# Optimization experiments

Measured on AMD Instinct MI355X. Metric: run time of the kernel, lower is better.

Reference implementation:

```python
import jax, jax.numpy as jnp
import numpy as np
import math

N_EMBD = 1024
N_HEAD = 16
N_CTX = 2048
SCALE = True
NEG = 1e10


def setup_inputs() -> dict:
    key = jax.random.key(0)
    ks = jax.random.split(key, 4)
    B, S = 2, 2048
    x = jax.random.normal(ks[0], (B, S, N_EMBD), dtype=jnp.float32)
    c_attn_w = jax.random.normal(ks[1], (N_EMBD, 3 * N_EMBD), dtype=jnp.float32) * 0.02
    c_attn_b = jnp.zeros((3 * N_EMBD,), dtype=jnp.float32)
    c_proj_w = jax.random.normal(ks[2], (N_EMBD, N_EMBD), dtype=jnp.float32) * 0.02
    c_proj_b = jnp.zeros((N_EMBD,), dtype=jnp.float32)
    return {"x": x, "c_attn_w": c_attn_w, "c_attn_b": c_attn_b,
            "c_proj_w": c_proj_w, "c_proj_b": c_proj_b}


def reference(x, c_attn_w, c_attn_b, c_proj_w, c_proj_b):
    B, S, D = x.shape
    H = N_HEAD
    hd = D // H
    qkv = x @ c_attn_w + c_attn_b                      # [B,S,3D]
    q, k, v = jnp.split(qkv, 3, axis=-1)
    # split heads -> [B,H,S,hd]
    q = q.reshape(B, S, H, hd).transpose(0, 2, 1, 3)
    k = k.reshape(B, S, H, hd).transpose(0, 2, 1, 3)
    v = v.reshape(B, S, H, hd).transpose(0, 2, 1, 3)
    w = jnp.einsum('bhqd,bhkd->bhqk', q, k)           # [B,H,S,S]
    if SCALE:
        w = w / math.sqrt(hd)
    # multiplicative causal mask trick: w*b - 1e10*(1-b)
    b = jnp.tril(jnp.ones((S, S), dtype=w.dtype))[None, None]
    w = w * b - NEG * (1.0 - b)
    w = jax.nn.softmax(w, axis=-1)
    a = jnp.einsum('bhqk,bhkd->bhqd', w, v)           # [B,H,S,hd]
    a = a.transpose(0, 2, 1, 3).reshape(B, S, D)      # merge heads
    a = a @ c_proj_w + c_proj_b
    present = jnp.stack((k, v))                       # [2,B,H,S,hd]
    return a, present
```

## Files before the change

kernel.cpp:

```cpp
#include <hip/hip_runtime.h>
#include <hip/hip_bf16.h>
#include <cstdint>
#include <cstddef>

#define SEQ 2048
#define DMODEL 1024
#define NHEAD 16
#define HDIM 64
#define MTOT 4096
#define NQKV 3072
#define KDIM 1024

#define OUT_K_BASE  4194304u
#define OUT_V_BASE  8388608u

#define QSCALE 0.18033688011112043f

typedef __attribute__((ext_vector_type(4))) float f32x4;
typedef __attribute__((ext_vector_type(8))) __bf16 bf16x8;
typedef __attribute__((ext_vector_type(8))) short s16x8;
typedef __attribute__((ext_vector_type(4))) short s16x4;
typedef __attribute__((ext_vector_type(2))) int i32x2;

static __device__ __forceinline__ unsigned short f2bf(float f) {
  unsigned int u = __builtin_bit_cast(unsigned int, f);
  u += 0x7FFFu + ((u >> 16) & 1u);
  return (unsigned short)(u >> 16);
}

static __device__ __forceinline__ float bf2f(unsigned short u) {
  unsigned int x = ((unsigned int)u) << 16;
  return __builtin_bit_cast(float, x);
}

static __device__ __forceinline__ s16x4 pack4(float4 v) {
  s16x4 r;
  r[0] = (short)f2bf(v.x);
  r[1] = (short)f2bf(v.y);
  r[2] = (short)f2bf(v.z);
  r[3] = (short)f2bf(v.w);
  return r;
}

static __device__ __forceinline__ int cvtpk(float lo, float hi) {
  int r;
  asm("v_cvt_pk_bf16_f32 %0, %1, %2" : "=v"(r) : "v"(lo), "v"(hi));
  return r;
}

static __device__ __forceinline__ f32x4 mfma16(s16x8 a, s16x8 b, f32x4 c) {
  return __builtin_amdgcn_mfma_f32_16x16x32_bf16(
      __builtin_bit_cast(bf16x8, a), __builtin_bit_cast(bf16x8, b), c, 0, 0, 0);
}

static __device__ __forceinline__ void gload16(const void* g, void* l) {
  __builtin_amdgcn_global_load_lds(
      (const __attribute__((address_space(1))) unsigned int*)(uintptr_t)g,
      (__attribute__((address_space(3))) unsigned int*)(uintptr_t)l,
      16, 0, 0);
}

#define WAITVM(n) asm volatile("s_waitcnt vmcnt(" #n ")" ::: "memory")

__global__ __launch_bounds__(256) void convert_x(
    const float* __restrict__ X, unsigned short* __restrict__ Xbf)
{
  int i = blockIdx.x * 256 + threadIdx.x;
  float4 v = reinterpret_cast<const float4*>(X)[i];
  reinterpret_cast<s16x4*>(Xbf)[i] = pack4(v);
}

__global__ __launch_bounds__(256) void convert_wt(
    const float* __restrict__ W, unsigned short* __restrict__ Wt, int N)
{
  __shared__ unsigned short t[64][72];
  const int n0 = blockIdx.x * 64, k0 = blockIdx.y * 64;
  const int tid = threadIdx.x;
#pragma unroll
  for (int i = 0; i < 4; ++i) {
    int f = tid + (i << 8);
    int r = f >> 4, c4 = (f & 15) << 2;
    float4 v = *reinterpret_cast<const float4*>(&W[(size_t)(k0 + r) * N + n0 + c4]);
    *reinterpret_cast<s16x4*>(&t[r][c4]) = pack4(v);
  }
  __syncthreads();
#pragma unroll
  for (int i = 0; i < 2; ++i) {
    int g = tid + (i << 8);
    int n = g >> 3, k8 = (g & 7) << 3;
    s16x8 o;
#pragma unroll
    for (int jj = 0; jj < 8; ++jj) o[jj] = (short)t[k8 + jj][n];
    *reinterpret_cast<s16x8*>(&Wt[(size_t)(n0 + n) * KDIM + k0 + k8]) = o;
  }
}

__global__ __launch_bounds__(256) void qkv_gemm(
    const unsigned short* __restrict__ Xbf,
    const unsigned short* __restrict__ Wt,
    const float* __restrict__ Bias,
    unsigned short* __restrict__ Qbf,
    unsigned short* __restrict__ Kbf,
    unsigned short* __restrict__ Vt)
{
  __shared__ __align__(16) unsigned short lds_a[2][128][64];
  __shared__ __align__(16) unsigned short lds_b[2][128][64];

  const int tid = threadIdx.x;
  const int lane = tid & 63;
  const int wv = tid >> 6;
  const int wr = wv >> 1, wc = wv & 1;
  const int m0 = blockIdx.x * 128;
  const int n0 = blockIdx.y * 128;
  const int lr = lane & 15;
  const int gq = lane >> 4;

  const f32x4 fzero = {0.f, 0.f, 0.f, 0.f};
  f32x4 acc[4][4];
#pragma unroll
  for (int i = 0; i < 4; ++i)
#pragma unroll
    for (int j = 0; j < 4; ++j) acc[i][j] = fzero;

  {
    const int r0 = tid >> 3;
    const int c0 = tid & 7;
    auto stage = [&](int nb, int kk) {
#pragma unroll
      for (int i = 0; i < 4; ++i) {
        int r = r0 + (i << 5);
        int sc = ((c0 ^ (r & 7)) << 3);
        int ub = (((i << 8) + (wv << 6)) << 3);
        gload16(&Xbf[(size_t)(m0 + r) * KDIM + kk + sc], &lds_a[nb][0][0] + ub);
        gload16(&Wt[(size_t)(n0 + r) * KDIM + kk + sc], &lds_b[nb][0][0] + ub);
      }
    };
    stage(0, 0);
    stage(1, 64);
    for (int t = 0; t < 16; ++t) {
      if (t < 15) { WAITVM(8); } else { WAITVM(0); }
      __builtin_amdgcn_s_barrier();
      const int bufg = t & 1;
      __builtin_amdgcn_s_setprio(1);
#pragma unroll
      for (int kf = 0; kf < 2; ++kf) {
        s16x8 bfv[4];
#pragma unroll
        for (int ni = 0; ni < 4; ++ni) {
          int row = wc * 64 + ni * 16 + lr;
          bfv[ni] = *reinterpret_cast<const s16x8*>(
              &lds_b[bufg][row][((kf * 4 + gq) ^ (row & 7)) << 3]);
        }
#pragma unroll
        for (int mi = 0; mi < 4; ++mi) {
          int row = wr * 64 + mi * 16 + lr;
          s16x8 af = *reinterpret_cast<const s16x8*>(
              &lds_a[bufg][row][((kf * 4 + gq) ^ (row & 7)) << 3]);
#pragma unroll
          for (int ni = 0; ni < 4; ++ni)
            acc[mi][ni] = mfma16(af, bfv[ni], acc[mi][ni]);
        }
      }
      __builtin_amdgcn_s_setprio(0);
      __builtin_amdgcn_s_barrier();
      if (t < 14) stage(bufg, (t + 2) << 6);
    }
  }

  __syncthreads();
  unsigned short* T = (wv < 2) ? (&lds_a[0][0][0] + (wv << 12))
                               : (&lds_b[0][0][0] + ((wv - 2) << 12));
  const int seg = n0 >> 10;
  const int b = m0 >> 11;
  const int s0 = (m0 & 2047) + wr * 64;
  const int h = ((n0 & 1023) >> 6) + wc;
  const size_t bh = (size_t)(b * NHEAD + h);

  if (seg <= 1) {
#pragma unroll
    for (int ni = 0; ni < 4; ++ni) {
      int c = n0 + wc * 64 + ni * 16 + lr;
      float bias = Bias[c];
      int ch = 2 * ni + (lr >> 3);
      int el = lr & 7;
#pragma unroll
      for (int mi = 0; mi < 4; ++mi)
#pragma unroll
        for (int j = 0; j < 4; ++j) {
          int s_loc = mi * 16 + gq * 4 + j;
          float val = acc[mi][ni][j] + bias;
          if (seg == 0) val *= QSCALE;
          T[s_loc * 64 + ((ch ^ (s_loc & 7)) << 3) + el] = f2bf(val);
        }
    }
    unsigned short* dst = (seg == 0) ? Qbf : Kbf;
#pragma unroll
    for (int it = 0; it < 8; ++it) {
      int rr = (lane >> 3) + (it << 3);
      int cl = lane & 7;
      s16x8 vv = *reinterpret_cast<const s16x8*>(
          &T[rr * 64 + ((cl ^ (rr & 7)) << 3)]);
      *reinterpret_cast<s16x8*>(
          &dst[(bh * SEQ + s0 + rr) * HDIM + (cl << 3)]) = vv;
    }
  } else {
#pragma unroll
    for (int ni = 0; ni < 4; ++ni) {
      int c = n0 + wc * 64 + ni * 16 + lr;
      float bias = Bias[c];
      int d_loc = ni * 16 + lr;
      int dsw = d_loc & 7;
#pragma unroll
      for (int mi = 0; mi < 4; ++mi)
#pragma unroll
        for (int j = 0; j < 4; ++j) {
          int s_loc = mi * 16 + gq * 4 + j;
          T[d_loc * 64 + (((s_loc >> 3) ^ dsw) << 3) + (s_loc & 7)] =
              f2bf(acc[mi][ni][j] + bias);
        }
    }
#pragma unroll
    for (int it = 0; it < 8; ++it) {
      int dl = (lane >> 3) + (it << 3);
      int cl = lane & 7;
      s16x8 vv = *reinterpret_cast<const s16x8*>(
          &T[dl * 64 + ((cl ^ (dl & 7)) << 3)]);
      *reinterpret_cast<s16x8*>(
          &Vt[(bh * HDIM + dl) * SEQ + s0 + (cl << 3)]) = vv;
    }
  }
}

__global__ __launch_bounds__(256) void expand_kv(
    const unsigned short* __restrict__ Kbf,
    const unsigned short* __restrict__ Vtg,
    float* __restrict__ out)
{
  __shared__ unsigned short T[64][72];
  const int tid = threadIdx.x;
  const int s0 = blockIdx.x * 64;
  const int bh = blockIdx.y;

#pragma unroll
  for (int i = 0; i < 2; ++i) {
    int idx = tid + (i << 8);
    int r = idx >> 3, dc = (idx & 7) << 3;
    size_t off = ((size_t)bh * SEQ + s0 + r) * HDIM + dc;
    s16x8 kv = *reinterpret_cast<const s16x8*>(&Kbf[off]);
    float4 lo = {bf2f((unsigned short)kv[0]), bf2f((unsigned short)kv[1]),
                 bf2f((unsigned short)kv[2]), bf2f((unsigned short)kv[3])};
    float4 hi = {bf2f((unsigned short)kv[4]), bf2f((unsigned short)kv[5]),
                 bf2f((unsigned short)kv[6]), bf2f((unsigned short)kv[7])};
    *reinterpret_cast<float4*>(&out[OUT_K_BASE + off]) = lo;
    *reinterpret_cast<float4*>(&out[OUT_K_BASE + off + 4]) = hi;
  }

#pragma unroll
  for (int i = 0; i < 2; ++i) {
    int idx = tid + (i << 8);
    int d = idx >> 3, sc = idx & 7;
    s16x8 vv = *reinterpret_cast<const s16x8*>(
        &Vtg[((size_t)bh * HDIM + d) * SEQ + s0 + (sc << 3)]);
#pragma unroll
    for (int e = 0; e < 8; ++e) T[sc * 8 + e][d] = (unsigned short)vv[e];
  }
  __syncthreads();
#pragma unroll
  for (int i = 0; i < 2; ++i) {
    int idx = tid + (i << 8);
    int sr = idx >> 3, dc = (idx & 7) << 3;
    s16x8 vv = *reinterpret_cast<const s16x8*>(&T[sr][dc]);
    float4 lo = {bf2f((unsigned short)vv[0]), bf2f((unsigned short)vv[1]),
                 bf2f((unsigned short)vv[2]), bf2f((unsigned short)vv[3])};
    float4 hi = {bf2f((unsigned short)vv[4]), bf2f((unsigned short)vv[5]),
                 bf2f((unsigned short)vv[6]), bf2f((unsigned short)vv[7])};
    size_t off = ((size_t)bh * SEQ + s0 + sr) * HDIM + dc;
    *reinterpret_cast<float4*>(&out[OUT_V_BASE + off]) = lo;
    *reinterpret_cast<float4*>(&out[OUT_V_BASE + off + 4]) = hi;
  }
}

__global__ __launch_bounds__(256) void proj_gemm(
    const unsigned short* __restrict__ Abf,
    const unsigned short* __restrict__ Wpt,
    const float* __restrict__ Bias,
    float* __restrict__ out)
{
  __shared__ __align__(16) unsigned short lds_a[2][128][64];
  __shared__ __align__(16) unsigned short lds_b[2][128][64];

  const int tid = threadIdx.x;
  const int lane = tid & 63;
  const int wv = tid >> 6;
  const int wr = wv >> 1, wc = wv & 1;
  const int m0 = blockIdx.x * 128;
  const int n0 = blockIdx.y * 128;
  const int lr = lane & 15;
  const int gq = lane >> 4;

  const f32x4 fzero = {0.f, 0.f, 0.f, 0.f};
  f32x4 acc[4][4];
#pragma unroll
  for (int i = 0; i < 4; ++i)
#pragma unroll
    for (int j = 0; j < 4; ++j) acc[i][j] = fzero;

  {
    const int r0 = tid >> 3;
    const int c0 = tid & 7;
    auto stage = [&](int nb, int kk) {
#pragma unroll
      for (int i = 0; i < 4; ++i) {
        int r = r0 + (i << 5);
        int sc = ((c0 ^ (r & 7)) << 3);
        int ub = (((i << 8) + (wv << 6)) << 3);
        gload16(&Abf[(size_t)(m0 + r) * KDIM + kk + sc], &lds_a[nb][0][0] + ub);
        gload16(&Wpt[(size_t)(n0 + r) * KDIM + kk + sc], &lds_b[nb][0][0] + ub);
      }
    };
    stage(0, 0);
    stage(1, 64);
    for (int t = 0; t < 16; ++t) {
      if (t < 15) { WAITVM(8); } else { WAITVM(0); }
      __builtin_amdgcn_s_barrier();
      const int bufg = t & 1;
      __builtin_amdgcn_s_setprio(1);
#pragma unroll
      for (int kf = 0; kf < 2; ++kf) {
        s16x8 bfv[4];
#pragma unroll
        for (int ni = 0; ni < 4; ++ni) {
          int row = wc * 64 + ni * 16 + lr;
          bfv[ni] = *reinterpret_cast<const s16x8*>(
              &lds_b[bufg][row][((kf * 4 + gq) ^ (row & 7)) << 3]);
        }
#pragma unroll
        for (int mi = 0; mi < 4; ++mi) {
          int row = wr * 64 + mi * 16 + lr;
          s16x8 af = *reinterpret_cast<const s16x8*>(
              &lds_a[bufg][row][((kf * 4 + gq) ^ (row & 7)) << 3]);
#pragma unroll
          for (int ni = 0; ni < 4; ++ni)
            acc[mi][ni] = mfma16(af, bfv[ni], acc[mi][ni]);
        }
      }
      __builtin_amdgcn_s_setprio(0);
      __builtin_amdgcn_s_barrier();
      if (t < 14) stage(bufg, (t + 2) << 6);
    }
  }

#pragma unroll
  for (int ni = 0; ni < 4; ++ni) {
    int c = n0 + wc * 64 + ni * 16 + lr;
    float bias = Bias[c];
#pragma unroll
    for (int mi = 0; mi < 4; ++mi) {
#pragma unroll
      for (int j = 0; j < 4; ++j) {
        int m = m0 + wr * 64 + mi * 16 + gq * 4 + j;
        out[(size_t)m * DMODEL + c] = acc[mi][ni][j] + bias;
      }
    }
  }
}

__global__ __launch_bounds__(256, 4) void attn_fwd(
    const unsigned short* __restrict__ Qbf,
    const unsigned short* __restrict__ Kbf,
    const unsigned short* __restrict__ Vtg,
    unsigned short* __restrict__ Abf)
{
  __shared__ __align__(16) unsigned short K_lds[2][64][64];
  __shared__ __align__(16) unsigned short V_lds[2][64][64];
  __shared__ __align__(16) unsigned short P_lds[4][16][64];

  const int tid = threadIdx.x;
  const int lane = tid & 63;
  const int wv = tid >> 6;
  const int bid = blockIdx.x;
  const int qt = 31 - (bid >> 5);
  const int bh = bid & 31;

  const int lr = lane & 15;
  const int gq = lane >> 4;

  const unsigned short* Kg = Kbf + (size_t)bh * (SEQ * HDIM);
  const unsigned short* Vg = Vtg + (size_t)bh * (SEQ * HDIM);
  const unsigned short* Qg = Qbf + (size_t)bh * (SEQ * HDIM)
                                 + (size_t)(qt * 64 + wv * 16) * HDIM;

  s16x8 qf0 = *reinterpret_cast<const s16x8*>(&Qg[lr * 64 + (gq << 3)]);
  s16x8 qf1 = *reinterpret_cast<const s16x8*>(&Qg[lr * 64 + 32 + (gq << 3)]);

  const f32x4 fzero = {0.f, 0.f, 0.f, 0.f};
  f32x4 O[4];
  float mrow = -1e30f, lrow = 0.f;
#pragma unroll
  for (int no = 0; no < 4; ++no) O[no] = fzero;

#define STAGE(kv0, nb)                                                        \
  {                                                                           \
    _Pragma("unroll")                                                         \
    for (int i = 0; i < 2; ++i) {                                             \
      int L = tid + (i << 8);                                                 \
      int r = L >> 3, c = L & 7;                                              \
      int cc = (c ^ (r & 7)) << 3;                                            \
      int ubase = ((i << 8) + (wv << 6)) << 3;                                \
      gload16(&Kg[(((kv0) + r) << 6) + cc], &K_lds[nb][0][0] + ubase);        \
      gload16(&Vg[((size_t)r << 11) + (kv0) + cc], &V_lds[nb][0][0] + ubase); \
    }                                                                         \
  }

  STAGE(0, 0);

  for (int t = 0; t <= qt; ++t) {
    __syncthreads();
    if (t < qt) STAGE((t + 1) * 64, (t + 1) & 1);
    const int buf = t & 1;

    f32x4 sc[4];
#pragma unroll
    for (int ni = 0; ni < 4; ++ni) {
      int kr = ni * 16 + lr;
      int sw = kr & 7;
      s16x8 kb0 = *reinterpret_cast<const s16x8*>(&K_lds[buf][kr][(gq ^ sw) << 3]);
      s16x8 kb1 = *reinterpret_cast<const s16x8*>(&K_lds[buf][kr][((gq + 4) ^ sw) << 3]);
      f32x4 tacc = mfma16(kb0, qf0, fzero);
      sc[ni] = mfma16(kb1, qf1, tacc);
    }

    if (t == qt) {
      int qloc = wv * 16 + lr;
#pragma unroll
      for (int ni = 0; ni < 4; ++ni)
#pragma unroll
        for (int r = 0; r < 4; ++r)
          if (ni * 16 + gq * 4 + r > qloc) sc[ni][r] = -1e30f;
    }

    float tmax = fmaxf(fmaxf(fmaxf(sc[0][0], sc[0][1]), fmaxf(sc[0][2], sc[0][3])),
                       fmaxf(fmaxf(sc[1][0], sc[1][1]), fmaxf(sc[1][2], sc[1][3])));
    tmax = fmaxf(tmax,
                 fmaxf(fmaxf(fmaxf(sc[2][0], sc[2][1]), fmaxf(sc[2][2], sc[2][3])),
                       fmaxf(fmaxf(sc[3][0], sc[3][1]), fmaxf(sc[3][2], sc[3][3]))));
    tmax = fmaxf(tmax, __shfl_xor(tmax, 16));
    tmax = fmaxf(tmax, __shfl_xor(tmax, 32));
    float newm = fmaxf(mrow, tmax);
    float fs = __builtin_amdgcn_exp2f(mrow - newm);
    mrow = newm;
    float rs = 0.f;
#pragma unroll
    for (int ni = 0; ni < 4; ++ni) {
#pragma unroll
      for (int r = 0; r < 4; ++r) {
        float p = __builtin_amdgcn_exp2f(sc[ni][r] - newm);
        sc[ni][r] = p;
        rs += p;
      }
    }
    rs += __shfl_xor(rs, 16);
    rs += __shfl_xor(rs, 32);
    lrow = lrow * fs + rs;
#pragma unroll
    for (int no = 0; no < 4; ++no) O[no] *= fs;

    {
      unsigned short* Prow = &P_lds[wv][lr][0];
      const int swl = lr & 7;
#pragma unroll
      for (int ni = 0; ni < 4; ++ni) {
        i32x2 d2;
        d2[0] = cvtpk(sc[ni][0], sc[ni][1]);
        d2[1] = cvtpk(sc[ni][2], sc[ni][3]);
        int off = ((((2 * ni) + (gq >> 1)) ^ swl) << 3) + ((gq & 1) << 2);
        *reinterpret_cast<i32x2*>(&Prow[off]) = d2;
      }
      s16x8 pB0 = *reinterpret_cast<const s16x8*>(&Prow[(gq ^ swl) << 3]);
      s16x8 pB1 = *reinterpret_cast<const s16x8*>(&Prow[((gq + 4) ^ swl) << 3]);

#pragma unroll
      for (int no = 0; no < 4; ++no) {
        int dr = no * 16 + lr;
        int sw = dr & 7;
        s16x8 vb0 = *reinterpret_cast<const s16x8*>(&V_lds[buf][dr][(gq ^ sw) << 3]);
        s16x8 vb1 = *reinterpret_cast<const s16x8*>(&V_lds[buf][dr][((gq + 4) ^ sw) << 3]);
        O[no] = mfma16(vb0, pB0, O[no]);
        O[no] = mfma16(vb1, pB1, O[no]);
      }
    }
  }

  const int b = bh >> 4, h = bh & 15;
  float inv = 1.0f / lrow;
  int srow = qt * 64 + wv * 16 + lr;
  size_t base = (size_t)(b * SEQ + srow) * DMODEL + h * 64 + (gq << 2);
#pragma unroll
  for (int no = 0; no < 4; ++no) {
    s16x4 ov;
#pragma unroll
    for (int r = 0; r < 4; ++r) ov[r] = (short)f2bf(O[no][r] * inv);
    *reinterpret_cast<s16x4*>(&Abf[base + no * 16]) = ov;
  }
#undef STAGE
}

extern "C" void kernel_launch(void* const* d_in, const int* in_sizes, int n_in,
                              void* d_out, int out_size, void* d_ws, size_t ws_size,
                              hipStream_t stream) {
  const float* x        = (const float*)d_in[0];
  const float* c_attn_w = (const float*)d_in[1];
  const float* c_attn_b = (const float*)d_in[2];
  const float* c_proj_w = (const float*)d_in[3];
  const float* c_proj_b = (const float*)d_in[4];
  float* out = (float*)d_out;

  unsigned short* Qbf = (unsigned short*)d_ws;
  unsigned short* Xbf = Qbf + 4194304;
  unsigned short* Abf = Xbf;
  unsigned short* Wt  = Qbf + 8388608;
  unsigned short* Wpt = Wt;
  unsigned short* Kbf = (unsigned short*)out;
  unsigned short* Vt  = Kbf + 4194304;

  convert_x<<<dim3(4096), 256, 0, stream>>>(x, Xbf);
  convert_wt<<<dim3(48, 16), 256, 0, stream>>>(c_attn_w, Wt, NQKV);
  qkv_gemm<<<dim3(32, 24), 256, 0, stream>>>(Xbf, Wt, c_attn_b, Qbf, Kbf, Vt);
  expand_kv<<<dim3(32, 32), 256, 0, stream>>>(Kbf, Vt, out);
  convert_wt<<<dim3(16, 16), 256, 0, stream>>>(c_proj_w, Wpt, DMODEL);
  attn_fwd<<<dim3(1024), 256, 0, stream>>>(Qbf, Kbf, Vt, Abf);
  proj_gemm<<<dim3(32, 8), 256, 0, stream>>>(Abf, Wpt, c_proj_b, out);
}
```

Baseline: 116.1 us.

## Fuse KV fp32 expansion into QKV GEMM epilogue and widen attention query tiles

The separate expand_kv kernel is removed. The QKV GEMM epilogue now writes the fp32 K and V copies of `present` directly from its registers and LDS tile, re-staging V in row-major order to do so. This avoids re-reading the bf16 K/V buffers and one kernel launch. The attention kernel now gives each block 128 query rows (each wave handles two 16-row groups), so each staged K/V tile is reused across twice as many queries, halving the block count. The trade-offs are higher register pressure (the 4-blocks-per-SM launch-bound hint is dropped), a coarser and possibly less balanced grid, and extra epilogue work and LDS traffic in the GEMM.

```diff
diff --git a/kernel.cpp b/kernel.cpp
--- a/kernel.cpp
+++ b/kernel.cpp
@@ -101,7 +101,8 @@
     const float* __restrict__ Bias,
     unsigned short* __restrict__ Qbf,
     unsigned short* __restrict__ Kbf,
-    unsigned short* __restrict__ Vt)
+    unsigned short* __restrict__ Vt,
+    float* __restrict__ outp)
 {
   __shared__ __align__(16) unsigned short lds_a[2][128][64];
   __shared__ __align__(16) unsigned short lds_b[2][128][64];
@@ -200,8 +201,16 @@
       int cl = lane & 7;
       s16x8 vv = *reinterpret_cast<const s16x8*>(
           &T[rr * 64 + ((cl ^ (rr & 7)) << 3)]);
-      *reinterpret_cast<s16x8*>(
-          &dst[(bh * SEQ + s0 + rr) * HDIM + (cl << 3)]) = vv;
+      size_t off = (bh * SEQ + s0 + rr) * HDIM + (cl << 3);
+      *reinterpret_cast<s16x8*>(&dst[off]) = vv;
+      if (seg == 1) {
+        float4 lo = {bf2f((unsigned short)vv[0]), bf2f((unsigned short)vv[1]),
+                     bf2f((unsigned short)vv[2]), bf2f((unsigned short)vv[3])};
+        float4 hi = {bf2f((unsigned short)vv[4]), bf2f((unsigned short)vv[5]),
+                     bf2f((unsigned short)vv[6]), bf2f((unsigned short)vv[7])};
+        *reinterpret_cast<float4*>(&outp[OUT_K_BASE + off]) = lo;
+        *reinterpret_cast<float4*>(&outp[OUT_K_BASE + off + 4]) = hi;
+      }
     }
   } else {
 #pragma unroll
@@ -228,55 +237,35 @@
       *reinterpret_cast<s16x8*>(
           &Vt[(bh * HDIM + dl) * SEQ + s0 + (cl << 3)]) = vv;
     }
-  }
-}
-
-__global__ __launch_bounds__(256) void expand_kv(
-    const unsigned short* __restrict__ Kbf,
-    const unsigned short* __restrict__ Vtg,
-    float* __restrict__ out)
-{
-  __shared__ unsigned short T[64][72];
-  const int tid = threadIdx.x;
-  const int s0 = blockIdx.x * 64;
-  const int bh = blockIdx.y;
-
-#pragma unroll
-  for (int i = 0; i < 2; ++i) {
-    int idx = tid + (i << 8);
-    int r = idx >> 3, dc = (idx & 7) << 3;
-    size_t off = ((size_t)bh * SEQ + s0 + r) * HDIM + dc;
-    s16x8 kv = *reinterpret_cast<const s16x8*>(&Kbf[off]);
-    float4 lo = {bf2f((unsigned short)kv[0]), bf2f((unsigned short)kv[1]),
-                 bf2f((unsigned short)kv[2]), bf2f((unsigned short)kv[3])};
-    float4 hi = {bf2f((unsigned short)kv[4]), bf2f((unsigned short)kv[5]),
-                 bf2f((unsigned short)kv[6]), bf2f((unsigned short)kv[7])};
-    *reinterpret_cast<float4*>(&out[OUT_K_BASE + off]) = lo;
-    *reinterpret_cast<float4*>(&out[OUT_K_BASE + off + 4]) = hi;
-  }
-
-#pragma unroll
-  for (int i = 0; i < 2; ++i) {
-    int idx = tid + (i << 8);
-    int d = idx >> 3, sc = idx & 7;
-    s16x8 vv = *reinterpret_cast<const s16x8*>(
-        &Vtg[((size_t)bh * HDIM + d) * SEQ + s0 + (sc << 3)]);
-#pragma unroll
-    for (int e = 0; e < 8; ++e) T[sc * 8 + e][d] = (unsigned short)vv[e];
-  }
-  __syncthreads();
-#pragma unroll
-  for (int i = 0; i < 2; ++i) {
-    int idx = tid + (i << 8);
-    int sr = idx >> 3, dc = (idx & 7) << 3;
-    s16x8 vv = *reinterpret_cast<const s16x8*>(&T[sr][dc]);
-    float4 lo = {bf2f((unsigned short)vv[0]), bf2f((unsigned short)vv[1]),
-                 bf2f((unsigned short)vv[2]), bf2f((unsigned short)vv[3])};
-    float4 hi = {bf2f((unsigned short)vv[4]), bf2f((unsigned short)vv[5]),
-                 bf2f((unsigned short)vv[6]), bf2f((unsigned short)vv[7])};
-    size_t off = ((size_t)bh * SEQ + s0 + sr) * HDIM + dc;
-    *reinterpret_cast<float4*>(&out[OUT_V_BASE + off]) = lo;
-    *reinterpret_cast<float4*>(&out[OUT_V_BASE + off + 4]) = hi;
+#pragma unroll
+    for (int ni = 0; ni < 4; ++ni) {
+      int c = n0 + wc * 64 + ni * 16 + lr;
+      float bias = Bias[c];
+      int ch = 2 * ni + (lr >> 3);
+      int el = lr & 7;
+#pragma unroll
+      for (int mi = 0; mi < 4; ++mi)
+#pragma unroll
+        for (int j = 0; j < 4; ++j) {
+          int s_loc = mi * 16 + gq * 4 + j;
+          T[s_loc * 64 + ((ch ^ (s_loc & 7)) << 3) + el] =
+              f2bf(acc[mi][ni][j] + bias);
+        }
+    }
+#pragma unroll
+    for (int it = 0; it < 8; ++it) {
+      int rr = (lane >> 3) + (it << 3);
+      int cl = lane & 7;
+      s16x8 vv = *reinterpret_cast<const s16x8*>(
+          &T[rr * 64 + ((cl ^ (rr & 7)) << 3)]);
+      float4 lo = {bf2f((unsigned short)vv[0]), bf2f((unsigned short)vv[1]),
+                   bf2f((unsigned short)vv[2]), bf2f((unsigned short)vv[3])};
+      float4 hi = {bf2f((unsigned short)vv[4]), bf2f((unsigned short)vv[5]),
+                   bf2f((unsigned short)vv[6]), bf2f((unsigned short)vv[7])};
+      size_t off = (bh * SEQ + s0 + rr) * HDIM + (cl << 3);
+      *reinterpret_cast<float4*>(&outp[OUT_V_BASE + off]) = lo;
+      *reinterpret_cast<float4*>(&outp[OUT_V_BASE + off + 4]) = hi;
+    }
   }
 }
 
@@ -365,7 +354,7 @@
   }
 }
 
-__global__ __launch_bounds__(256, 4) void attn_fwd(
+__global__ __launch_bounds__(256) void attn_fwd(
     const unsigned short* __restrict__ Qbf,
     const unsigned short* __restrict__ Kbf,
     const unsigned short* __restrict__ Vtg,
@@ -379,7 +368,7 @@
   const int lane = tid & 63;
   const int wv = tid >> 6;
   const int bid = blockIdx.x;
-  const int qt = 31 - (bid >> 5);
+  const int qt = 15 - (bid >> 5);
   const int bh = bid & 31;
 
   const int lr = lane & 15;
@@ -388,16 +377,22 @@
   const unsigned short* Kg = Kbf + (size_t)bh * (SEQ * HDIM);
   const unsigned short* Vg = Vtg + (size_t)bh * (SEQ * HDIM);
   const unsigned short* Qg = Qbf + (size_t)bh * (SEQ * HDIM)
-                                 + (size_t)(qt * 64 + wv * 16) * HDIM;
-
-  s16x8 qf0 = *reinterpret_cast<const s16x8*>(&Qg[lr * 64 + (gq << 3)]);
-  s16x8 qf1 = *reinterpret_cast<const s16x8*>(&Qg[lr * 64 + 32 + (gq << 3)]);
+                                 + (size_t)(qt * 128 + wv * 32) * HDIM;
+
+  s16x8 qf0[2], qf1[2];
+#pragma unroll
+  for (int g = 0; g < 2; ++g) {
+    qf0[g] = *reinterpret_cast<const s16x8*>(&Qg[(g * 16 + lr) * 64 + (gq << 3)]);
+    qf1[g] = *reinterpret_cast<const s16x8*>(&Qg[(g * 16 + lr) * 64 + 32 + (gq << 3)]);
+  }
 
   const f32x4 fzero = {0.f, 0.f, 0.f, 0.f};
-  f32x4 O[4];
-  float mrow = -1e30f, lrow = 0.f;
-#pragma unroll
-  for (int no = 0; no < 4; ++no) O[no] = fzero;
+  f32x4 O[2][4];
+  float mrow[2] = {-1e30f, -1e30f}, lrow[2] = {0.f, 0.f};
+#pragma unroll
+  for (int g = 0; g < 2; ++g)
+#pragma unroll
+    for (int no = 0; no < 4; ++no) O[g][no] = fzero;
 
 #define STAGE(kv0, nb)                                                        \
   {                                                                           \
@@ -412,95 +407,104 @@
     }                                                                         \
   }
 
+  const int ntiles = qt * 2 + 2;
   STAGE(0, 0);
 
-  for (int t = 0; t <= qt; ++t) {
+  for (int t = 0; t < ntiles; ++t) {
     __syncthreads();
-    if (t < qt) STAGE((t + 1) * 64, (t + 1) & 1);
+    if (t < ntiles - 1) STAGE((t + 1) * 64, (t + 1) & 1);
     const int buf = t & 1;
-
-    f32x4 sc[4];
-#pragma unroll
-    for (int ni = 0; ni < 4; ++ni) {
-      int kr = ni * 16 + lr;
-      int sw = kr & 7;
-      s16x8 kb0 = *reinterpret_cast<const s16x8*>(&K_lds[buf][kr][(gq ^ sw) << 3]);
-      s16x8 kb1 = *reinterpret_cast<const s16x8*>(&K_lds[buf][kr][((gq + 4) ^ sw) << 3]);
-      f32x4 tacc = mfma16(kb0, qf0, fzero);
-      sc[ni] = mfma16(kb1, qf1, tacc);
-    }
-
-    if (t == qt) {
-      int qloc = wv * 16 + lr;
-#pragma unroll
-      for (int ni = 0; ni < 4; ++ni)
-#pragma unroll
-        for (int r = 0; r < 4; ++r)
-          if (ni * 16 + gq * 4 + r > qloc) sc[ni][r] = -1e30f;
-    }
-
-    float tmax = fmaxf(fmaxf(fmaxf(sc[0][0], sc[0][1]), fmaxf(sc[0][2], sc[0][3])),
-                       fmaxf(fmaxf(sc[1][0], sc[1][1]), fmaxf(sc[1][2], sc[1][3])));
-    tmax = fmaxf(tmax,
-                 fmaxf(fmaxf(fmaxf(sc[2][0], sc[2][1]), fmaxf(sc[2][2], sc[2][3])),
-                       fmaxf(fmaxf(sc[3][0], sc[3][1]), fmaxf(sc[3][2], sc[3][3]))));
-    tmax = fmaxf(tmax, __shfl_xor(tmax, 16));
-    tmax = fmaxf(tmax, __shfl_xor(tmax, 32));
-    float newm = fmaxf(mrow, tmax);
-    float fs = __builtin_amdgcn_exp2f(mrow - newm);
-    mrow = newm;
-    float rs = 0.f;
-#pragma unroll
-    for (int ni = 0; ni < 4; ++ni) {
-#pragma unroll
-      for (int r = 0; r < 4; ++r) {
-        float p = __builtin_amdgcn_exp2f(sc[ni][r] - newm);
-        sc[ni][r] = p;
-        rs += p;
-      }
-    }
-    rs += __shfl_xor(rs, 16);
-    rs += __shfl_xor(rs, 32);
-    lrow = lrow * fs + rs;
-#pragma unroll
-    for (int no = 0; no < 4; ++no) O[no] *= fs;
-
-    {
-      unsigned short* Prow = &P_lds[wv][lr][0];
-      const int swl = lr & 7;
+    const bool needmask = (t >= 2 * qt);
+
+#pragma unroll
+    for (int g = 0; g < 2; ++g) {
+      f32x4 sc[4];
 #pragma unroll
       for (int ni = 0; ni < 4; ++ni) {
-        i32x2 d2;
-        d2[0] = cvtpk(sc[ni][0], sc[ni][1]);
-        d2[1] = cvtpk(sc[ni][2], sc[ni][3]);
-        int off = ((((2 * ni) + (gq >> 1)) ^ swl) << 3) + ((gq & 1) << 2);
-        *reinterpret_cast<i32x2*>(&Prow[off]) = d2;
-      }
-      s16x8 pB0 = *reinterpret_cast<const s16x8*>(&Prow[(gq ^ swl) << 3]);
-      s16x8 pB1 = *reinterpret_cast<const s16x8*>(&Prow[((gq + 4) ^ swl) << 3]);
-
-#pragma unroll
-      for (int no = 0; no < 4; ++no) {
-        int dr = no * 16 + lr;
-        int sw = dr & 7;
-        s16x8 vb0 = *reinterpret_cast<const s16x8*>(&V_lds[buf][dr][(gq ^ sw) << 3]);
-        s16x8 vb1 = *reinterpret_cast<const s16x8*>(&V_lds[buf][dr][((gq + 4) ^ sw) << 3]);
-        O[no] = mfma16(vb0, pB0, O[no]);
-        O[no] = mfma16(vb1, pB1, O[no]);
+        int kr = ni * 16 + lr;
+        int sw = kr & 7;
+        s16x8 kb0 = *reinterpret_cast<const s16x8*>(&K_lds[buf][kr][(gq ^ sw) << 3]);
+        s16x8 kb1 = *reinterpret_cast<const s16x8*>(&K_lds[buf][kr][((gq + 4) ^ sw) << 3]);
+        f32x4 tacc = mfma16(kb0, qf0[g], fzero);
+        sc[ni] = mfma16(kb1, qf1[g], tacc);
+      }
+
+      if (needmask) {
+        int qgl = qt * 128 + wv * 32 + g * 16 + lr;
+        int kvb = t * 64;
+#pragma unroll
+        for (int ni = 0; ni < 4; ++ni)
+#pragma unroll
+          for (int r = 0; r < 4; ++r)
+            if (kvb + ni * 16 + gq * 4 + r > qgl) sc[ni][r] = -1e30f;
+      }
+
+      float tmax = fmaxf(fmaxf(fmaxf(sc[0][0], sc[0][1]), fmaxf(sc[0][2], sc[0][3])),
+                         fmaxf(fmaxf(sc[1][0], sc[1][1]), fmaxf(sc[1][2], sc[1][3])));
+      tmax = fmaxf(tmax,
+                   fmaxf(fmaxf(fmaxf(sc[2][0], sc[2][1]), fmaxf(sc[2][2], sc[2][3])),
+                         fmaxf(fmaxf(sc[3][0], sc[3][1]), fmaxf(sc[3][2], sc[3][3]))));
+      tmax = fmaxf(tmax, __shfl_xor(tmax, 16));
+      tmax = fmaxf(tmax, __shfl_xor(tmax, 32));
+      float newm = fmaxf(mrow[g], tmax);
+      float fs = __builtin_amdgcn_exp2f(mrow[g] - newm);
+      mrow[g] = newm;
+      float rs = 0.f;
+#pragma unroll
+      for (int ni = 0; ni < 4; ++ni) {
+#pragma unroll
+        for (int r = 0; r < 4; ++r) {
+          float p = __builtin_amdgcn_exp2f(sc[ni][r] - newm);
+          sc[ni][r] = p;
+          rs += p;
+        }
+      }
+      rs += __shfl_xor(rs, 16);
+      rs += __shfl_xor(rs, 32);
+      lrow[g] = lrow[g] * fs + rs;
+#pragma unroll
+      for (int no = 0; no < 4; ++no) O[g][no] *= fs;
+
+      {
+        unsigned short* Prow = &P_lds[wv][lr][0];
+        const int swl = lr & 7;
+#pragma unroll
+        for (int ni = 0; ni < 4; ++ni) {
+          i32x2 d2;
+          d2[0] = cvtpk(sc[ni][0], sc[ni][1]);
+          d2[1] = cvtpk(sc[ni][2], sc[ni][3]);
+          int off = ((((2 * ni) + (gq >> 1)) ^ swl) << 3) + ((gq & 1) << 2);
+          *reinterpret_cast<i32x2*>(&Prow[off]) = d2;
+        }
+        s16x8 pB0 = *reinterpret_cast<const s16x8*>(&Prow[(gq ^ swl) << 3]);
+        s16x8 pB1 = *reinterpret_cast<const s16x8*>(&Prow[((gq + 4) ^ swl) << 3]);
+
+#pragma unroll
+        for (int no = 0; no < 4; ++no) {
+          int dr = no * 16 + lr;
+          int sw = dr & 7;
+          s16x8 vb0 = *reinterpret_cast<const s16x8*>(&V_lds[buf][dr][(gq ^ sw) << 3]);
+          s16x8 vb1 = *reinterpret_cast<const s16x8*>(&V_lds[buf][dr][((gq + 4) ^ sw) << 3]);
+          O[g][no] = mfma16(vb0, pB0, O[g][no]);
+          O[g][no] = mfma16(vb1, pB1, O[g][no]);
+        }
       }
     }
   }
 
   const int b = bh >> 4, h = bh & 15;
-  float inv = 1.0f / lrow;
-  int srow = qt * 64 + wv * 16 + lr;
-  size_t base = (size_t)(b * SEQ + srow) * DMODEL + h * 64 + (gq << 2);
-#pragma unroll
-  for (int no = 0; no < 4; ++no) {
-    s16x4 ov;
-#pragma unroll
-    for (int r = 0; r < 4; ++r) ov[r] = (short)f2bf(O[no][r] * inv);
-    *reinterpret_cast<s16x4*>(&Abf[base + no * 16]) = ov;
+#pragma unroll
+  for (int g = 0; g < 2; ++g) {
+    float inv = 1.0f / lrow[g];
+    int srow = qt * 128 + wv * 32 + g * 16 + lr;
+    size_t base = (size_t)(b * SEQ + srow) * DMODEL + h * 64 + (gq << 2);
+#pragma unroll
+    for (int no = 0; no < 4; ++no) {
+      s16x4 ov;
+#pragma unroll
+      for (int r = 0; r < 4; ++r) ov[r] = (short)f2bf(O[g][no][r] * inv);
+      *reinterpret_cast<s16x4*>(&Abf[base + no * 16]) = ov;
+    }
   }
 #undef STAGE
 }
@@ -525,9 +529,8 @@
 
   convert_x<<<dim3(4096), 256, 0, stream>>>(x, Xbf);
   convert_wt<<<dim3(48, 16), 256, 0, stream>>>(c_attn_w, Wt, NQKV);
-  qkv_gemm<<<dim3(32, 24), 256, 0, stream>>>(Xbf, Wt, c_attn_b, Qbf, Kbf, Vt);
-  expand_kv<<<dim3(32, 32), 256, 0, stream>>>(Kbf, Vt, out);
+  qkv_gemm<<<dim3(32, 24), 256, 0, stream>>>(Xbf, Wt, c_attn_b, Qbf, Kbf, Vt, out);
   convert_wt<<<dim3(16, 16), 256, 0, stream>>>(c_proj_w, Wpt, DMODEL);
-  attn_fwd<<<dim3(1024), 256, 0, stream>>>(Qbf, Kbf, Vt, Abf);
+  attn_fwd<<<dim3(512), 256, 0, stream>>>(Qbf, Kbf, Vt, Abf);
   proj_gemm<<<dim3(32, 8), 256, 0, stream>>>(Abf, Wpt, c_proj_b, out);
 }
```

New measurement: 129.9 us. 1.12x slower.
